# Performance work log

Hardware: AMD Instinct MI355X
Metric: run time of the kernel (lower is better)

The kernel has to match this reference:

```python
import jax, jax.numpy as jnp
import numpy as np

HIDDEN = 4096
NUM_HEADS = 32
HEAD_DIM = HIDDEN // NUM_HEADS  # 128
ROPE_THETA = 10000.0
B, S = 1, 2048


def setup_inputs() -> dict:
    key = jax.random.key(0)
    k1, k2, k3, k4, k5 = jax.random.split(key, 5)
    positions = jnp.broadcast_to(jnp.arange(S, dtype=jnp.int64), (B, S))
    hidden_states = jax.random.normal(k1, (B, S, HIDDEN), dtype=jnp.float32)
    scale = 1.0 / np.sqrt(HIDDEN)
    Wqkv = jax.random.normal(k2, (HIDDEN, 3 * HIDDEN), dtype=jnp.float32) * scale
    bqkv = jax.random.normal(k3, (3 * HIDDEN,), dtype=jnp.float32) * 0.01
    Wo = jax.random.normal(k4, (HIDDEN, HIDDEN), dtype=jnp.float32) * scale
    bo = jax.random.normal(k5, (HIDDEN,), dtype=jnp.float32) * 0.01
    return {"positions": positions, "hidden_states": hidden_states,
            "Wqkv": Wqkv, "bqkv": bqkv, "Wo": Wo, "bo": bo}


def _apply_rope(x, positions):
    # x: [B, S, H, D]; neox-style (rotate halves) rotary embedding
    half = HEAD_DIM // 2
    inv_freq = 1.0 / (ROPE_THETA ** (jnp.arange(0, HEAD_DIM, 2, dtype=jnp.float32) / HEAD_DIM))
    freqs = positions.astype(jnp.float32)[..., None] * inv_freq  # [B, S, half]
    cos = jnp.cos(freqs)[:, :, None, :]  # [B, S, 1, half]
    sin = jnp.sin(freqs)[:, :, None, :]
    x1, x2 = x[..., :half], x[..., half:]
    return jnp.concatenate([x1 * cos - x2 * sin, x2 * cos + x1 * sin], axis=-1)


def reference(positions, hidden_states, Wqkv, bqkv, Wo, bo):
    qkv = hidden_states @ Wqkv + bqkv  # [B, S, 3*HIDDEN]
    q, k, v = jnp.split(qkv, 3, axis=-1)
    q = q.reshape(B, S, NUM_HEADS, HEAD_DIM)
    k = k.reshape(B, S, NUM_HEADS, HEAD_DIM)
    v = v.reshape(B, S, NUM_HEADS, HEAD_DIM)
    q = _apply_rope(q, positions)
    k = _apply_rope(k, positions)
    scaling = HEAD_DIM ** -0.5
    scores = jnp.einsum('bshd,bthd->bhst', q, k) * scaling  # [B, H, S, S]
    causal = jnp.tril(jnp.ones((S, S), dtype=bool))
    scores = jnp.where(causal, scores, jnp.finfo(scores.dtype).min)
    attn = jax.nn.softmax(scores, axis=-1)
    out = jnp.einsum('bhst,bthd->bshd', attn, v).reshape(B, S, HIDDEN)
    return out @ Wo + bo
```

## Files before the change

kernel.cpp:

```cpp
#include <hip/hip_runtime.h>

using short8  = __attribute__((ext_vector_type(8))) short;
using floatx4 = __attribute__((ext_vector_type(4))) float;

__device__ inline float b2f(ushort u) {
  union { unsigned u; float f; } x; x.u = ((unsigned)u) << 16; return x.f;
}
__device__ inline ushort f2b(float f) {
  union { float f; unsigned u; } x; x.f = f;
  unsigned r = x.u + 0x7fffu + ((x.u >> 16) & 1u);
  return (ushort)(r >> 16);
}

__device__ __forceinline__ void gl_lds16(const void* g, void* l) {
  __builtin_amdgcn_global_load_lds(
      (const __attribute__((address_space(1))) unsigned*)(unsigned long long)g,
      (__attribute__((address_space(3))) unsigned*)(unsigned)(unsigned long long)l,
      16, 0, 0);
}

__global__ __launch_bounds__(256) void cvt_f32_bf16(
    const float* __restrict__ in, ushort* __restrict__ out, int n4) {
  const int i = blockIdx.x * 256 + threadIdx.x;
  if (i < n4) {
    const float4 v = ((const float4*)in)[i];
    ushort4 o;
    o.x = f2b(v.x); o.y = f2b(v.y); o.z = f2b(v.z); o.w = f2b(v.w);
    ((ushort4*)out)[i] = o;
  }
}

__global__ __launch_bounds__(256) void transpose_f32_bf16(
    const float* __restrict__ W, int ldw, ushort* __restrict__ Wt, int K) {
  __shared__ ushort tile[64 * 64];
  const int kb = blockIdx.y * 64, nb = blockIdx.x * 64;
  const int t = threadIdx.x;
  {
    const int tn4 = t & 15;
    const int tk  = t >> 4;
#pragma unroll
    for (int i = 0; i < 4; ++i) {
      const int k = tk + i * 16;
      const float4 v = *(const float4*)&W[(size_t)(kb + k) * ldw + nb + tn4 * 4];
      ushort4 o; o.x = f2b(v.x); o.y = f2b(v.y); o.z = f2b(v.z); o.w = f2b(v.w);
      const int c = tn4 ^ (k & 15);
      *(ushort4*)&tile[k * 64 + c * 4] = o;
    }
  }
  __syncthreads();
  {
    const int kc = t & 7;
    const int tn = t >> 3;
#pragma unroll
    for (int p = 0; p < 2; ++p) {
      const int n = tn + p * 32;
      union { int4 v; ushort u[8]; } o;
#pragma unroll
      for (int j = 0; j < 8; ++j) {
        const int k = kc * 8 + j;
        const int c = (n >> 2) ^ (k & 15);
        o.u[j] = tile[k * 64 + c * 4 + (n & 3)];
      }
      *(int4*)&Wt[(size_t)(nb + n) * K + kb + kc * 8] = o.v;
    }
  }
}

__global__ __launch_bounds__(256) void transpose_v_bf16(
    const ushort* __restrict__ qkv, ushort* __restrict__ vT) {
  __shared__ ushort tile[64 * 64];
  const int s0 = blockIdx.y * 64, c0 = blockIdx.x * 64;
  const int t = threadIdx.x;
  {
    const int tc8 = t & 7, ts = t >> 3;
#pragma unroll
    for (int p = 0; p < 2; ++p) {
      const int s = ts + p * 32;
      int4 x = *(const int4*)(qkv + (size_t)(s0 + s) * 12288 + 8192 + c0 + tc8 * 8);
      const int c8 = tc8 ^ (s & 7) ^ ((s >> 3) & 7);
      *(int4*)&tile[s * 64 + c8 * 8] = x;
    }
  }
  __syncthreads();
  {
    const int sc = t & 7, tc = t >> 3;
#pragma unroll
    for (int p = 0; p < 2; ++p) {
      const int c = tc + p * 32;
      union { int4 v; ushort u[8]; } o;
#pragma unroll
      for (int j = 0; j < 8; ++j) {
        const int s = sc * 8 + j;
        const int c8 = (c >> 3) ^ (s & 7) ^ ((s >> 3) & 7);
        o.u[j] = tile[s * 64 + c8 * 8 + (c & 7)];
      }
      *(int4*)&vT[(size_t)(c0 + c) * 2048 + s0 + sc * 8] = o.v;
    }
  }
}

template <bool F32OUT>
__global__ __launch_bounds__(256) void gemm_bt_bias(
    const ushort* __restrict__ A, const ushort* __restrict__ Bt,
    const float* __restrict__ bias, void* __restrict__ Cout,
    int ldc, int M, int N, int K) {
  __shared__ ushort sA[128 * 64];
  __shared__ ushort sB[128 * 64];
  const int tid = threadIdx.x;
  const int lane = tid & 63, w = tid >> 6;
  const int lm = lane & 15, lq = lane >> 4;
  const int wr = w >> 1, wc = w & 1;
  const int m0 = blockIdx.y * 128, n0 = blockIdx.x * 128;
  floatx4 acc[4][4] = {};

  const int srow = w * 32 + (lane >> 3);
  const int scol = (lane & 7) * 8;
  const ushort* Ag = A + (size_t)(m0 + srow) * K + scol;
  const ushort* Bg = Bt + (size_t)(n0 + srow) * K + scol;

  for (int k0 = 0; k0 < K; k0 += 64) {
    __syncthreads();
#pragma unroll
    for (int j = 0; j < 4; ++j) {
      gl_lds16(Ag + (size_t)j * 8 * K + k0, &sA[(w * 32 + j * 8) * 64]);
      gl_lds16(Bg + (size_t)j * 8 * K + k0, &sB[(w * 32 + j * 8) * 64]);
    }
    __syncthreads();
#pragma unroll
    for (int ks = 0; ks < 2; ++ks) {
      short8 af[4], bf[4];
#pragma unroll
      for (int i = 0; i < 4; ++i)
        af[i] = *(const short8*)&sA[(wr * 64 + i * 16 + lm) * 64 + ks * 32 + lq * 8];
#pragma unroll
      for (int j = 0; j < 4; ++j)
        bf[j] = *(const short8*)&sB[(wc * 64 + j * 16 + lm) * 64 + ks * 32 + lq * 8];
#pragma unroll
      for (int i = 0; i < 4; ++i)
#pragma unroll
        for (int j = 0; j < 4; ++j)
          acc[i][j] = __builtin_amdgcn_mfma_f32_16x16x32_bf16(af[i], bf[j], acc[i][j], 0, 0, 0);
    }
  }
#pragma unroll
  for (int i = 0; i < 4; ++i) {
#pragma unroll
    for (int j = 0; j < 4; ++j) {
      const int row = m0 + wr * 64 + i * 16 + lq * 4;
      const int col = n0 + wc * 64 + j * 16 + lm;
      const float bs = bias[col];
      if (F32OUT) {
        float* C = (float*)Cout;
#pragma unroll
        for (int r = 0; r < 4; ++r)
          C[(size_t)(row + r) * ldc + col] = acc[i][j][r] + bs;
      } else {
        ushort* C = (ushort*)Cout;
#pragma unroll
        for (int r = 0; r < 4; ++r)
          C[(size_t)(row + r) * ldc + col] = f2b(acc[i][j][r] + bs);
      }
    }
  }
}

__global__ __launch_bounds__(256) void rope_kernel(ushort* __restrict__ qkv) {
  const int s = blockIdx.x;
  const float pos = (float)s;
  const int t = threadIdx.x;
  const int h = t >> 3, d8 = (t & 7) * 8;
  const size_t base = (size_t)s * 12288 + h * 128 + d8;
  union U { int4 v; ushort u[8]; };
  U q1, q2, k1, k2;
  q1.v = *(const int4*)(qkv + base);
  q2.v = *(const int4*)(qkv + base + 64);
  k1.v = *(const int4*)(qkv + base + 4096);
  k2.v = *(const int4*)(qkv + base + 4160);
  float sn[8], cs[8];
#pragma unroll
  for (int j = 0; j < 8; ++j) {
    const float inv_freq = exp2f(-(float)(d8 + j) * 0.20762050593045952f);
    sincosf(pos * inv_freq, &sn[j], &cs[j]);
  }
  U o1, o2;
#pragma unroll
  for (int j = 0; j < 8; ++j) {
    const float x1 = b2f(q1.u[j]), x2 = b2f(q2.u[j]);
    o1.u[j] = f2b(x1 * cs[j] - x2 * sn[j]);
    o2.u[j] = f2b(x2 * cs[j] + x1 * sn[j]);
  }
  *(int4*)(qkv + base)      = o1.v;
  *(int4*)(qkv + base + 64) = o2.v;
#pragma unroll
  for (int j = 0; j < 8; ++j) {
    const float x1 = b2f(k1.u[j]), x2 = b2f(k2.u[j]);
    o1.u[j] = f2b(x1 * cs[j] - x2 * sn[j]);
    o2.u[j] = f2b(x2 * cs[j] + x1 * sn[j]);
  }
  *(int4*)(qkv + base + 4096) = o1.v;
  *(int4*)(qkv + base + 4160) = o2.v;
}

__global__ __launch_bounds__(256) void flash_kernel(
    const ushort* __restrict__ qkv, const ushort* __restrict__ vT,
    ushort* __restrict__ attn) {
  constexpr int QKV = 12288;
  __shared__ ushort smem[20480];
  ushort* sK  = smem;
  ushort* sVt = smem + 8192;
  ushort* sP  = smem + 16384;

  const int h   = blockIdx.y;
  const int tid = threadIdx.x;
  const int lane = tid & 63, w = tid >> 6;
  const int lm = lane & 15, lq = lane >> 4;
  const int c16 = lane & 15, l4 = lane >> 4;
  const int c8  = lane & 7,  l3 = lane >> 3;
  const float sc = 0.08838834764831845f * 1.4426950408889634f;

  const int qt = 31 - blockIdx.x;
  const int q0 = qt * 64;

#pragma unroll
  for (int j = 0; j < 4; ++j) {
    const int row = w * 16 + j * 4 + l4;
    const int sw = c16 ^ (row & 7);
    gl_lds16(qkv + (size_t)(q0 + row) * QKV + h * 128 + sw * 8,
             &sK[(w * 16 + j * 4) * 128]);
  }
  __syncthreads();
  short8 aq[4];
#pragma unroll
  for (int kk = 0; kk < 4; ++kk)
    aq[kk] = *(const short8*)&sK[(w * 16 + lm) * 128 + (((kk * 4 + lq) ^ (lm & 7)) * 8)];

  floatx4 acco[8] = {};
  float mrun[4], lrun[4];
#pragma unroll
  for (int r = 0; r < 4; ++r) { mrun[r] = -1e30f; lrun[r] = 0.f; }

  const int nkv = qt + 1;
  for (int it = 0; it < nkv; ++it) {
    const int kv0 = it * 64;
    __syncthreads();
#pragma unroll
    for (int j = 0; j < 4; ++j) {
      const int row = w * 16 + j * 4 + l4;
      const int sw = c16 ^ (row & 7);
      gl_lds16(qkv + (size_t)(kv0 + row) * QKV + 4096 + h * 128 + sw * 8,
               &sK[(w * 16 + j * 4) * 128]);
    }
#pragma unroll
    for (int j = 0; j < 4; ++j) {
      const int vrow = w * 32 + j * 8 + l3;
      const int sw = c8 ^ (vrow & 7);
      gl_lds16(vT + (size_t)(h * 128 + vrow) * 2048 + kv0 + sw * 8,
               &sVt[(w * 32 + j * 8) * 64]);
    }
    __syncthreads();

    floatx4 accs[4] = {};
#pragma unroll
    for (int kk = 0; kk < 4; ++kk) {
      short8 bk[4];
#pragma unroll
      for (int nt = 0; nt < 4; ++nt)
        bk[nt] = *(const short8*)&sK[(nt * 16 + lm) * 128 + (((kk * 4 + lq) ^ (lm & 7)) * 8)];
#pragma unroll
      for (int nt = 0; nt < 4; ++nt)
        accs[nt] = __builtin_amdgcn_mfma_f32_16x16x32_bf16(aq[kk], bk[nt], accs[nt], 0, 0, 0);
    }

    const bool domask = (it == nkv - 1);
    float tmax[4];
#pragma unroll
    for (int r = 0; r < 4; ++r) tmax[r] = -1e30f;
#pragma unroll
    for (int nt = 0; nt < 4; ++nt)
#pragma unroll
      for (int r = 0; r < 4; ++r) {
        float v = accs[nt][r] * sc;
        if (domask) {
          const int qrow = q0 + w * 16 + lq * 4 + r;
          const int kcol = kv0 + nt * 16 + lm;
          if (kcol > qrow) v = -1e30f;
        }
        accs[nt][r] = v;
        tmax[r] = fmaxf(tmax[r], v);
      }
#pragma unroll
    for (int r = 0; r < 4; ++r) {
      float t = tmax[r];
#pragma unroll
      for (int off = 1; off < 16; off <<= 1) t = fmaxf(t, __shfl_xor(t, off, 64));
      const float mnew = fmaxf(mrun[r], t);
      const float alpha = exp2f(mrun[r] - mnew);
      mrun[r] = mnew;
      lrun[r] *= alpha;
#pragma unroll
      for (int nt = 0; nt < 8; ++nt) acco[nt][r] *= alpha;
    }
    float rsum[4] = {};
#pragma unroll
    for (int nt = 0; nt < 4; ++nt)
#pragma unroll
      for (int r = 0; r < 4; ++r) {
        const float p = exp2f(accs[nt][r] - mrun[r]);
        rsum[r] += p;
        sP[(w * 16 + lq * 4 + r) * 64 +
           (((2 * nt + (lm >> 3)) ^ ((lq * 4 + r) & 7)) * 8) + (lm & 7)] = f2b(p);
      }
#pragma unroll
    for (int r = 0; r < 4; ++r) {
      float t = rsum[r];
#pragma unroll
      for (int off = 1; off < 16; off <<= 1) t += __shfl_xor(t, off, 64);
      lrun[r] += t;
    }

#pragma unroll
    for (int ks = 0; ks < 2; ++ks) {
      const short8 ap = *(const short8*)&sP[(w * 16 + lm) * 64 + (((ks * 4 + lq) ^ (lm & 7)) * 8)];
#pragma unroll
      for (int nt = 0; nt < 8; ++nt) {
        const short8 bv = *(const short8*)&sVt[(nt * 16 + lm) * 64 + (((ks * 4 + lq) ^ (lm & 7)) * 8)];
        acco[nt] = __builtin_amdgcn_mfma_f32_16x16x32_bf16(ap, bv, acco[nt], 0, 0, 0);
      }
    }
  }

#pragma unroll
  for (int r = 0; r < 4; ++r) {
    const float inv = 1.0f / lrun[r];
    const int row = q0 + w * 16 + lq * 4 + r;
#pragma unroll
    for (int nt = 0; nt < 8; ++nt) {
      const int col = h * 128 + nt * 16 + lm;
      attn[(size_t)row * 4096 + col] = f2b(acco[nt][r] * inv);
    }
  }
}

extern "C" void kernel_launch(void* const* d_in, const int* in_sizes, int n_in,
                              void* d_out, int out_size, void* d_ws, size_t ws_size,
                              hipStream_t stream) {
  const float* hidden = (const float*)d_in[1];
  const float* Wqkv   = (const float*)d_in[2];
  const float* bqkv   = (const float*)d_in[3];
  const float* Wo     = (const float*)d_in[4];
  const float* bo     = (const float*)d_in[5];

  ushort* ws   = (ushort*)d_ws;
  ushort* Wt   = ws;
  ushort* hb   = ws + (size_t)16777216;
  ushort* qkv  = ws + (size_t)25165824;
  ushort* attn = ws + (size_t)50331648;

  cvt_f32_bf16<<<8192, 256, 0, stream>>>(hidden, hb, 2097152);

  for (int c = 0; c < 3; ++c) {
    transpose_f32_bf16<<<dim3(64, 64), 256, 0, stream>>>(Wqkv + c * 4096, 12288, Wt, 4096);
    gemm_bt_bias<false><<<dim3(32, 16), 256, 0, stream>>>(
        hb, Wt, bqkv + c * 4096, (void*)(qkv + c * 4096), 12288, 2048, 4096, 4096);
  }

  rope_kernel<<<2048, 256, 0, stream>>>(qkv);
  transpose_v_bf16<<<dim3(64, 32), 256, 0, stream>>>(qkv, Wt);
  flash_kernel<<<dim3(32, 32), 256, 0, stream>>>(qkv, Wt, attn);

  transpose_f32_bf16<<<dim3(64, 64), 256, 0, stream>>>(Wo, 4096, Wt, 4096);
  gemm_bt_bias<true><<<dim3(32, 16), 256, 0, stream>>>(
      attn, Wt, bo, d_out, 4096, 2048, 4096, 4096);
}
```

Measured before the change: 942.1 us.

## Double-buffer flash K/V loads, pair causal q-tiles, fuse QKV GEMM launch

The flash kernel now double-buffers K and V tiles in LDS, prefetching the next tile while computing on the current one. Each block handles two complementary q-tiles (qt and 31-qt) so the causal workload is balanced, which halves the grid. The online-softmax rescale is skipped when no row max increases. When the workspace is large enough, the three per-chunk QKV transposes and GEMMs become one full-width transpose and GEMM. These add more LDS per block and fewer blocks, which may lower occupancy.

```diff
diff --git a/kernel.cpp b/kernel.cpp
--- a/kernel.cpp
+++ b/kernel.cpp
@@ -205,10 +205,8 @@
     const ushort* __restrict__ qkv, const ushort* __restrict__ vT,
     ushort* __restrict__ attn) {
   constexpr int QKV = 12288;
-  __shared__ ushort smem[20480];
-  ushort* sK  = smem;
-  ushort* sVt = smem + 8192;
-  ushort* sP  = smem + 16384;
+  __shared__ ushort smem[36864];
+  ushort* sP = smem + 32768;
 
   const int h   = blockIdx.y;
   const int tid = threadIdx.x;
@@ -218,125 +216,161 @@
   const int c8  = lane & 7,  l3 = lane >> 3;
   const float sc = 0.08838834764831845f * 1.4426950408889634f;
 
-  const int qt = 31 - blockIdx.x;
-  const int q0 = qt * 64;
-
-#pragma unroll
-  for (int j = 0; j < 4; ++j) {
-    const int row = w * 16 + j * 4 + l4;
-    const int sw = c16 ^ (row & 7);
-    gl_lds16(qkv + (size_t)(q0 + row) * QKV + h * 128 + sw * 8,
-             &sK[(w * 16 + j * 4) * 128]);
-  }
-  __syncthreads();
-  short8 aq[4];
-#pragma unroll
-  for (int kk = 0; kk < 4; ++kk)
-    aq[kk] = *(const short8*)&sK[(w * 16 + lm) * 128 + (((kk * 4 + lq) ^ (lm & 7)) * 8)];
-
-  floatx4 acco[8] = {};
-  float mrun[4], lrun[4];
-#pragma unroll
-  for (int r = 0; r < 4; ++r) { mrun[r] = -1e30f; lrun[r] = 0.f; }
-
-  const int nkv = qt + 1;
-  for (int it = 0; it < nkv; ++it) {
-    const int kv0 = it * 64;
+  for (int qsel = 0; qsel < 2; ++qsel) {
+    const int qt = qsel ? (int)blockIdx.x : 31 - (int)blockIdx.x;
+    const int q0 = qt * 64;
+    const int nkv = qt + 1;
+
     __syncthreads();
 #pragma unroll
     for (int j = 0; j < 4; ++j) {
       const int row = w * 16 + j * 4 + l4;
       const int sw = c16 ^ (row & 7);
-      gl_lds16(qkv + (size_t)(kv0 + row) * QKV + 4096 + h * 128 + sw * 8,
-               &sK[(w * 16 + j * 4) * 128]);
+      gl_lds16(qkv + (size_t)(q0 + row) * QKV + h * 128 + sw * 8,
+               &smem[8192 + (w * 16 + j * 4) * 128]);
+    }
+#pragma unroll
+    for (int j = 0; j < 4; ++j) {
+      const int row = w * 16 + j * 4 + l4;
+      const int sw = c16 ^ (row & 7);
+      gl_lds16(qkv + (size_t)row * QKV + 4096 + h * 128 + sw * 8,
+               &smem[(w * 16 + j * 4) * 128]);
     }
 #pragma unroll
     for (int j = 0; j < 4; ++j) {
       const int vrow = w * 32 + j * 8 + l3;
       const int sw = c8 ^ (vrow & 7);
-      gl_lds16(vT + (size_t)(h * 128 + vrow) * 2048 + kv0 + sw * 8,
-               &sVt[(w * 32 + j * 8) * 64]);
+      gl_lds16(vT + (size_t)(h * 128 + vrow) * 2048 + sw * 8,
+               &smem[16384 + (w * 32 + j * 8) * 64]);
     }
     __syncthreads();
-
-    floatx4 accs[4] = {};
-#pragma unroll
-    for (int kk = 0; kk < 4; ++kk) {
-      short8 bk[4];
+    short8 aq[4];
+#pragma unroll
+    for (int kk = 0; kk < 4; ++kk)
+      aq[kk] = *(const short8*)&smem[8192 + (w * 16 + lm) * 128 + (((kk * 4 + lq) ^ (lm & 7)) * 8)];
+    __syncthreads();
+
+    floatx4 acco[8] = {};
+    float mrun[4], lrun[4];
+#pragma unroll
+    for (int r = 0; r < 4; ++r) { mrun[r] = -1e30f; lrun[r] = 0.f; }
+
+    for (int it = 0; it < nkv; ++it) {
+      const int cur = it & 1;
+      ushort* dK = smem + cur * 8192;
+      ushort* dV = smem + 16384 + cur * 8192;
+
+      if (it + 1 < nkv) {
+        const int kv1 = (it + 1) * 64;
+        ushort* pK = smem + (cur ^ 1) * 8192;
+        ushort* pV = smem + 16384 + (cur ^ 1) * 8192;
+#pragma unroll
+        for (int j = 0; j < 4; ++j) {
+          const int row = w * 16 + j * 4 + l4;
+          const int sw = c16 ^ (row & 7);
+          gl_lds16(qkv + (size_t)(kv1 + row) * QKV + 4096 + h * 128 + sw * 8,
+                   &pK[(w * 16 + j * 4) * 128]);
+        }
+#pragma unroll
+        for (int j = 0; j < 4; ++j) {
+          const int vrow = w * 32 + j * 8 + l3;
+          const int sw = c8 ^ (vrow & 7);
+          gl_lds16(vT + (size_t)(h * 128 + vrow) * 2048 + kv1 + sw * 8,
+                   &pV[(w * 32 + j * 8) * 64]);
+        }
+      }
+
+      const int kv0 = it * 64;
+      floatx4 accs[4] = {};
+#pragma unroll
+      for (int kk = 0; kk < 4; ++kk) {
+        short8 bk[4];
+#pragma unroll
+        for (int nt = 0; nt < 4; ++nt)
+          bk[nt] = *(const short8*)&dK[(nt * 16 + lm) * 128 + (((kk * 4 + lq) ^ (lm & 7)) * 8)];
+#pragma unroll
+        for (int nt = 0; nt < 4; ++nt)
+          accs[nt] = __builtin_amdgcn_mfma_f32_16x16x32_bf16(aq[kk], bk[nt], accs[nt], 0, 0, 0);
+      }
+
+      const bool domask = (it == nkv - 1);
+      float tmax[4];
+#pragma unroll
+      for (int r = 0; r < 4; ++r) tmax[r] = -1e30f;
 #pragma unroll
       for (int nt = 0; nt < 4; ++nt)
-        bk[nt] = *(const short8*)&sK[(nt * 16 + lm) * 128 + (((kk * 4 + lq) ^ (lm & 7)) * 8)];
+#pragma unroll
+        for (int r = 0; r < 4; ++r) {
+          float v = accs[nt][r] * sc;
+          if (domask) {
+            const int qrow = q0 + w * 16 + lq * 4 + r;
+            const int kcol = kv0 + nt * 16 + lm;
+            if (kcol > qrow) v = -1e30f;
+          }
+          accs[nt][r] = v;
+          tmax[r] = fmaxf(tmax[r], v);
+        }
+      float tr[4];
+#pragma unroll
+      for (int r = 0; r < 4; ++r) {
+        float t = tmax[r];
+#pragma unroll
+        for (int off = 1; off < 16; off <<= 1) t = fmaxf(t, __shfl_xor(t, off, 64));
+        tr[r] = t;
+      }
+      unsigned long long need = 0;
+#pragma unroll
+      for (int r = 0; r < 4; ++r) need |= __ballot(tr[r] > mrun[r]);
+      if (need) {
+#pragma unroll
+        for (int r = 0; r < 4; ++r) {
+          const float mnew = fmaxf(mrun[r], tr[r]);
+          const float alpha = exp2f(mrun[r] - mnew);
+          mrun[r] = mnew;
+          lrun[r] *= alpha;
+#pragma unroll
+          for (int nt = 0; nt < 8; ++nt) acco[nt][r] *= alpha;
+        }
+      }
+      float rsum[4] = {};
 #pragma unroll
       for (int nt = 0; nt < 4; ++nt)
-        accs[nt] = __builtin_amdgcn_mfma_f32_16x16x32_bf16(aq[kk], bk[nt], accs[nt], 0, 0, 0);
-    }
-
-    const bool domask = (it == nkv - 1);
-    float tmax[4];
-#pragma unroll
-    for (int r = 0; r < 4; ++r) tmax[r] = -1e30f;
-#pragma unroll
-    for (int nt = 0; nt < 4; ++nt)
+#pragma unroll
+        for (int r = 0; r < 4; ++r) {
+          const float p = exp2f(accs[nt][r] - mrun[r]);
+          rsum[r] += p;
+          sP[(w * 16 + lq * 4 + r) * 64 +
+             (((2 * nt + (lm >> 3)) ^ ((lq * 4 + r) & 7)) * 8) + (lm & 7)] = f2b(p);
+        }
 #pragma unroll
       for (int r = 0; r < 4; ++r) {
-        float v = accs[nt][r] * sc;
-        if (domask) {
-          const int qrow = q0 + w * 16 + lq * 4 + r;
-          const int kcol = kv0 + nt * 16 + lm;
-          if (kcol > qrow) v = -1e30f;
-        }
-        accs[nt][r] = v;
-        tmax[r] = fmaxf(tmax[r], v);
-      }
+        float t = rsum[r];
+#pragma unroll
+        for (int off = 1; off < 16; off <<= 1) t += __shfl_xor(t, off, 64);
+        lrun[r] += t;
+      }
+
+#pragma unroll
+      for (int ks = 0; ks < 2; ++ks) {
+        const short8 ap = *(const short8*)&sP[(w * 16 + lm) * 64 + (((ks * 4 + lq) ^ (lm & 7)) * 8)];
+#pragma unroll
+        for (int nt = 0; nt < 8; ++nt) {
+          const short8 bv = *(const short8*)&dV[(nt * 16 + lm) * 64 + (((ks * 4 + lq) ^ (lm & 7)) * 8)];
+          acco[nt] = __builtin_amdgcn_mfma_f32_16x16x32_bf16(ap, bv, acco[nt], 0, 0, 0);
+        }
+      }
+      __syncthreads();
+    }
+
 #pragma unroll
     for (int r = 0; r < 4; ++r) {
-      float t = tmax[r];
-#pragma unroll
-      for (int off = 1; off < 16; off <<= 1) t = fmaxf(t, __shfl_xor(t, off, 64));
-      const float mnew = fmaxf(mrun[r], t);
-      const float alpha = exp2f(mrun[r] - mnew);
-      mrun[r] = mnew;
-      lrun[r] *= alpha;
-#pragma unroll
-      for (int nt = 0; nt < 8; ++nt) acco[nt][r] *= alpha;
-    }
-    float rsum[4] = {};
-#pragma unroll
-    for (int nt = 0; nt < 4; ++nt)
-#pragma unroll
-      for (int r = 0; r < 4; ++r) {
-        const float p = exp2f(accs[nt][r] - mrun[r]);
-        rsum[r] += p;
-        sP[(w * 16 + lq * 4 + r) * 64 +
-           (((2 * nt + (lm >> 3)) ^ ((lq * 4 + r) & 7)) * 8) + (lm & 7)] = f2b(p);
-      }
-#pragma unroll
-    for (int r = 0; r < 4; ++r) {
-      float t = rsum[r];
-#pragma unroll
-      for (int off = 1; off < 16; off <<= 1) t += __shfl_xor(t, off, 64);
-      lrun[r] += t;
-    }
-
-#pragma unroll
-    for (int ks = 0; ks < 2; ++ks) {
-      const short8 ap = *(const short8*)&sP[(w * 16 + lm) * 64 + (((ks * 4 + lq) ^ (lm & 7)) * 8)];
+      const float inv = 1.0f / lrun[r];
+      const int row = q0 + w * 16 + lq * 4 + r;
 #pragma unroll
       for (int nt = 0; nt < 8; ++nt) {
-        const short8 bv = *(const short8*)&sVt[(nt * 16 + lm) * 64 + (((ks * 4 + lq) ^ (lm & 7)) * 8)];
-        acco[nt] = __builtin_amdgcn_mfma_f32_16x16x32_bf16(ap, bv, acco[nt], 0, 0, 0);
-      }
-    }
-  }
-
-#pragma unroll
-  for (int r = 0; r < 4; ++r) {
-    const float inv = 1.0f / lrun[r];
-    const int row = q0 + w * 16 + lq * 4 + r;
-#pragma unroll
-    for (int nt = 0; nt < 8; ++nt) {
-      const int col = h * 128 + nt * 16 + lm;
-      attn[(size_t)row * 4096 + col] = f2b(acco[nt][r] * inv);
+        const int col = h * 128 + nt * 16 + lm;
+        attn[(size_t)row * 4096 + col] = f2b(acco[nt][r] * inv);
+      }
     }
   }
 }
@@ -351,22 +385,29 @@
   const float* bo     = (const float*)d_in[5];
 
   ushort* ws   = (ushort*)d_ws;
-  ushort* Wt   = ws;
-  ushort* hb   = ws + (size_t)16777216;
-  ushort* qkv  = ws + (size_t)25165824;
-  ushort* attn = ws + (size_t)50331648;
+  ushort* hb   = ws;
+  ushort* qkv  = ws + (size_t)8388608;
+  ushort* attn = ws + (size_t)33554432;
+  ushort* Wt   = ws + (size_t)41943040;
 
   cvt_f32_bf16<<<8192, 256, 0, stream>>>(hidden, hb, 2097152);
 
-  for (int c = 0; c < 3; ++c) {
-    transpose_f32_bf16<<<dim3(64, 64), 256, 0, stream>>>(Wqkv + c * 4096, 12288, Wt, 4096);
-    gemm_bt_bias<false><<<dim3(32, 16), 256, 0, stream>>>(
-        hb, Wt, bqkv + c * 4096, (void*)(qkv + c * 4096), 12288, 2048, 4096, 4096);
+  const bool fused = ws_size >= (size_t)184549376;
+  if (fused) {
+    transpose_f32_bf16<<<dim3(192, 64), 256, 0, stream>>>(Wqkv, 12288, Wt, 4096);
+    gemm_bt_bias<false><<<dim3(96, 16), 256, 0, stream>>>(
+        hb, Wt, bqkv, (void*)qkv, 12288, 2048, 12288, 4096);
+  } else {
+    for (int c = 0; c < 3; ++c) {
+      transpose_f32_bf16<<<dim3(64, 64), 256, 0, stream>>>(Wqkv + c * 4096, 12288, Wt, 4096);
+      gemm_bt_bias<false><<<dim3(32, 16), 256, 0, stream>>>(
+          hb, Wt, bqkv + c * 4096, (void*)(qkv + c * 4096), 12288, 2048, 4096, 4096);
+    }
   }
 
   rope_kernel<<<2048, 256, 0, stream>>>(qkv);
   transpose_v_bf16<<<dim3(64, 32), 256, 0, stream>>>(qkv, Wt);
-  flash_kernel<<<dim3(32, 32), 256, 0, stream>>>(qkv, Wt, attn);
+  flash_kernel<<<dim3(16, 32), 256, 0, stream>>>(qkv, Wt, attn);
 
   transpose_f32_bf16<<<dim3(64, 64), 256, 0, stream>>>(Wo, 4096, Wt, 4096);
   gemm_bt_bias<true><<<dim3(32, 16), 256, 0, stream>>>(
```

Measured after the change: 900.0 us. 1.05x faster.
